# Optimization experiments

Hardware: AMD Instinct MI355X
Metric: run time of the kernel (lower is better)

The kernel has to match this reference:

```python
import jax, jax.numpy as jnp
import numpy as np

FACTOR = 5  # sampling factor from __init__


def setup_inputs() -> dict:
    key = jax.random.key(0)
    k1, k2, k3, k4 = jax.random.split(key, 4)
    B, L, H, D = 4, 2048, 8, 64
    S = min(FACTOR * int(np.ceil(np.log(L))), L)  # U_part = 40
    return {
        "queries": jax.random.normal(k1, (B, L, H, D), jnp.float32),
        "keys": jax.random.normal(k2, (B, L, H, D), jnp.float32),
        "values": jax.random.normal(k3, (B, L, H, D), jnp.float32),
        "index_sample": jax.random.randint(k4, (L, S), 0, L, jnp.int32),
    }


def reference(queries, keys, values, index_sample):
    B, L_Q, H, D = queries.shape
    L_K = keys.shape[1]
    Q = jnp.transpose(queries, (0, 2, 1, 3))  # [B,H,L_Q,D]
    K = jnp.transpose(keys, (0, 2, 1, 3))     # [B,H,L_K,D]
    V = jnp.transpose(values, (0, 2, 1, 3))   # [B,H,L_K,D]

    u = min(FACTOR * int(np.ceil(np.log(L_Q))), L_Q)  # n_top

    # --- _prob_QK: sampled QK to score queries, then top-u query selection ---
    # K_sample[b,h,q,s,:] = K[b,h,index_sample[q,s],:]  -> [B,H,L_Q,S,D]
    K_sample = K[:, :, index_sample, :]
    Q_K_sample = jnp.einsum('bhqd,bhqsd->bhqs', Q, K_sample)  # [B,H,L_Q,S]
    M = Q_K_sample.max(-1) - Q_K_sample.sum(-1) / L_K         # sparsity measure
    _, M_top = jax.lax.top_k(M, u)                            # [B,H,u] query indices

    Q_reduce = jnp.take_along_axis(Q, M_top[..., None], axis=2)  # [B,H,u,D]
    scale = 1.0 / np.sqrt(D)
    scores = jnp.einsum('bhud,bhkd->bhuk', Q_reduce, K) * scale  # [B,H,u,L_K]

    # --- _update_context causal mask: rows are the FIRST u rows of the full
    # triu(L_Q,L_Q) mask (faithful to original, which does NOT reindex by M_top)
    causal = jnp.triu(jnp.ones((u, L_Q), dtype=bool), 1)
    scores = jnp.where(causal[None, None], -jnp.inf, scores)
    attn = jax.nn.softmax(scores, axis=-1)
    upd = jnp.einsum('bhuk,bhkd->bhud', attn, V)  # [B,H,u,D]

    # --- _get_initial_context (mask_flag=True): running cumsum of V ---
    context = jnp.cumsum(V, axis=2)  # [B,H,L_Q,D]

    # scatter-overwrite selected query positions
    b = jnp.arange(B)[:, None, None]
    h = jnp.arange(H)[None, :, None]
    context = context.at[b, h, M_top].set(upd)

    return jnp.transpose(context, (0, 2, 1, 3))  # [B,L_Q,H,D]
```

## Files before the change

### kernel.cpp

```cpp
#include <hip/hip_runtime.h>
#include <stdint.h>

constexpr int B = 4;
constexpr int L = 2048;
constexpr int H = 8;
constexpr int D = 64;
constexpr int S = 40;
constexpr int U = 40;
constexpr int HD = H * D;
constexpr int NSEG = 8;
constexpr int SEGL = L / NSEG;
constexpr int NC = 64;
constexpr int CL = L / NC;

__device__ __forceinline__ unsigned mono(float v) {
    unsigned u = __float_as_uint(v);
    return (u & 0x80000000u) ? ~u : (u | 0x80000000u);
}

typedef float f4v __attribute__((ext_vector_type(4)));

__device__ __forceinline__ float4 ntload4(const float4* p) {
    f4v v = __builtin_nontemporal_load((const f4v*)p);
    return make_float4(v.x, v.y, v.z, v.w);
}

__global__ __launch_bounds__(256) void k_scores(
    const float4* __restrict__ Q4, const float4* __restrict__ K4,
    const int* __restrict__ idxs, float* __restrict__ M)
{
    int i = blockIdx.x;
    int xcd = i & 7;
    int b = xcd >> 1;
    int qc = (i >> 3) * 2 + (xcd & 1);
    int w = threadIdx.x >> 6;
    int lane = threadIdx.x & 63;
    int q = qc * 4 + w;
    int h = lane >> 3;
    int dd = lane & 7;

    const float4* qrow = Q4 + (size_t)(b * L + q) * 128;
    float4 qa = ntload4(qrow + 2 * lane);
    float4 qb = ntload4(qrow + 2 * lane + 1);

    int v_idx = idxs[q * S + (lane < S ? lane : 0)];

    const float4* kbase = K4 + (size_t)b * L * 128;
    float mx = -INFINITY, sm = 0.f;
    #pragma unroll 8
    for (int s = 0; s < S; ++s) {
        int ki = __shfl(v_idx, s);
        const float4* krow = kbase + (size_t)ki * 128;
        float4 ka = krow[2 * lane], kb = krow[2 * lane + 1];
        float d = qa.x * ka.x + qa.y * ka.y + qa.z * ka.z + qa.w * ka.w
                + qb.x * kb.x + qb.y * kb.y + qb.z * kb.z + qb.w * kb.w;
        d += __shfl_xor(d, 1);
        d += __shfl_xor(d, 2);
        d += __shfl_xor(d, 4);
        mx = fmaxf(mx, d);
        sm += d;
    }
    if (dd == 0)
        M[(b * 8 + h) * L + q] = mx - sm * (1.0f / (float)L);
}

__global__ __launch_bounds__(512) void k_topk_attn(
    const float* __restrict__ M, const float4* __restrict__ Q4,
    const float4* __restrict__ K4, const float4* __restrict__ V4,
    int* __restrict__ flags, float* __restrict__ upd)
{
    __shared__ unsigned long long cnd[NSEG * U];
    __shared__ int top_idx[U];
    __shared__ __align__(16) float Qs[U * 68];
    __shared__ __align__(16) float Kst[64 * 65];
    __shared__ __align__(16) float Vs[U * 68];
    __shared__ __align__(16) float Plds[U * 44];

    int bh = blockIdx.x;
    int b = bh >> 3, h = bh & 7;
    int tid = threadIdx.x;
    int wv = tid >> 6, lane = tid & 63;

    int seg = wv;
    int j0 = seg * SEGL + lane * 4;

    *(int4*)(flags + (size_t)bh * L + j0) = make_int4(0, 0, 0, 0);

    float4 v = *(const float4*)(M + (size_t)bh * L + j0);
    unsigned m[4] = { mono(v.x), mono(v.y), mono(v.z), mono(v.w) };
    int rank[4] = { 0, 0, 0, 0 };

    #pragma unroll 4
    for (int src = 0; src < 64; ++src) {
        #pragma unroll
        for (int slot = 0; slot < 4; ++slot) {
            unsigned bm = __shfl(m[slot], src);
            int bj = src * 4 + slot;
            #pragma unroll
            for (int s = 0; s < 4; ++s) {
                int myj = lane * 4 + s;
                rank[s] += (bm > m[s]) || (bm == m[s] && bj < myj);
            }
        }
    }
    #pragma unroll
    for (int s = 0; s < 4; ++s)
        if (rank[s] < U)
            cnd[seg * U + rank[s]] = ((unsigned long long)m[s] << 32)
                                   | (unsigned)(~(unsigned)(j0 + s));
    __syncthreads();

    if (tid < NSEG * U) {
        unsigned long long ka = cnd[tid];
        int ra = 0;
        #pragma unroll 8
        for (int j = 0; j < NSEG * U; ++j) ra += (cnd[j] > ka);
        if (ra < U) top_idx[ra] = (int)(~(unsigned)ka);
    }
    __syncthreads();

    if (tid < U) flags[bh * L + top_idx[tid]] = tid + 1;

    for (int i = tid; i < U * 16; i += 512) {
        int r = i >> 4, d4 = i & 15;
        size_t kvbase = ((size_t)(b * L + r) * H + h) * 16 + d4;
        float4 kv = K4[kvbase];
        Kst[(4 * d4 + 0) * 65 + r] = kv.x;
        Kst[(4 * d4 + 1) * 65 + r] = kv.y;
        Kst[(4 * d4 + 2) * 65 + r] = kv.z;
        Kst[(4 * d4 + 3) * 65 + r] = kv.w;
        *(float4*)(Vs + r * 68 + d4 * 4) = V4[kvbase];
        *(float4*)(Qs + r * 68 + d4 * 4) =
            Q4[((size_t)(b * L + top_idx[r]) * H + h) * 16 + d4];
    }
    __syncthreads();

    const float scale = 0.125f;
    int k = lane;
    for (int rr = 0; rr < 5; ++rr) {
        int r = wv * 5 + rr;
        float acc = 0.f;
        #pragma unroll
        for (int d0 = 0; d0 < D; d0 += 4) {
            float4 qv = *(const float4*)(Qs + r * 68 + d0);
            acc += qv.x * Kst[(d0 + 0) * 65 + k];
            acc += qv.y * Kst[(d0 + 1) * 65 + k];
            acc += qv.z * Kst[(d0 + 2) * 65 + k];
            acc += qv.w * Kst[(d0 + 3) * 65 + k];
        }
        float sc = (k <= r) ? acc * scale : -INFINITY;
        float mx = sc;
        #pragma unroll
        for (int off = 32; off >= 1; off >>= 1)
            mx = fmaxf(mx, __shfl_xor(mx, off));
        float e = __expf(sc - mx);
        float sum = e;
        #pragma unroll
        for (int off = 32; off >= 1; off >>= 1)
            sum += __shfl_xor(sum, off);
        float p = e / sum;
        if (k < U) Plds[r * 44 + k] = p;
    }
    __syncthreads();

    for (int t = tid; t < U * D; t += 512) {
        int r = t >> 6, d = t & 63;
        float acc = 0.f;
        #pragma unroll
        for (int kk = 0; kk < U; kk += 4) {
            float4 pv = *(const float4*)(Plds + r * 44 + kk);
            acc += pv.x * Vs[(kk + 0) * 68 + d];
            acc += pv.y * Vs[(kk + 1) * 68 + d];
            acc += pv.z * Vs[(kk + 2) * 68 + d];
            acc += pv.w * Vs[(kk + 3) * 68 + d];
        }
        upd[((size_t)bh * U + r) * D + d] = acc;
    }
}

__global__ __launch_bounds__(512) void k_chunksum(
    const float* __restrict__ V, float* __restrict__ partial)
{
    int b = blockIdx.x >> 6;
    int c = blockIdx.x & 63;
    int hd = threadIdx.x;
    const float* vp = V + ((size_t)(b * L + c * CL)) * HD + hd;
    float s = 0.f;
    #pragma unroll
    for (int l = 0; l < CL; ++l) s += vp[(size_t)l * HD];
    partial[((size_t)b * NC + c) * HD + hd] = s;
}

__global__ __launch_bounds__(512) void k_out(
    const float* __restrict__ V, const float* __restrict__ partial,
    const int* __restrict__ flags, const float* __restrict__ upd,
    float* __restrict__ out)
{
    int b = blockIdx.x >> 6;
    int c = blockIdx.x & 63;
    int hd = threadIdx.x;
    int h = hd >> 6, d = hd & 63;

    float acc = 0.f;
    const float* pp = partial + (size_t)b * NC * HD + hd;
    for (int j = 0; j < c; ++j) acc += pp[(size_t)j * HD];

    const float* vp = V + ((size_t)(b * L + c * CL)) * HD + hd;
    float*       op = out + ((size_t)(b * L + c * CL)) * HD + hd;
    const int*   fp = flags + (b * H + h) * L + c * CL;
    const float* up = upd + (size_t)(b * H + h) * U * D + d;

    #pragma unroll 4
    for (int l = 0; l < CL; ++l) {
        acc += vp[(size_t)l * HD];
        int f = fp[l];
        float o = f ? up[(size_t)(f - 1) * D] : acc;
        __builtin_nontemporal_store(o, op + (size_t)l * HD);
    }
}

extern "C" void kernel_launch(void* const* d_in, const int* in_sizes, int n_in,
                              void* d_out, int out_size, void* d_ws, size_t ws_size,
                              hipStream_t stream)
{
    const float* Q   = (const float*)d_in[0];
    const float* K   = (const float*)d_in[1];
    const float* V   = (const float*)d_in[2];
    const int*  idxs = (const int*)d_in[3];
    float* out = (float*)d_out;

    char* ws = (char*)d_ws;
    float* M        = (float*)(ws);
    int*   flags    = (int*)  (ws + 262144);
    float* upd      = (float*)(ws + 524288);
    float* partial  = (float*)(ws + 851968);

    k_scores    <<<B * L / 4, 256, 0, stream>>>((const float4*)Q, (const float4*)K, idxs, M);
    k_topk_attn <<<B * H,     512, 0, stream>>>(M, (const float4*)Q, (const float4*)K,
                                                (const float4*)V, flags, upd);
    k_chunksum  <<<B * NC,    512, 0, stream>>>(V, partial);
    k_out       <<<B * NC,    512, 0, stream>>>(V, partial, flags, upd, out);
}
```

Before: 182.4 us.

## Fuse chunk-sum and flag clearing into scores kernel; split top-k across blocks

Merges the V chunk-sum and the flag-zeroing into the scoring kernel's grid as extra block ranges, so those independent jobs run alongside scoring instead of in a later launch. The per-segment rank-based top-k selection moves out of the 32-block attention kernel into its own kernel with 256 small blocks, which writes candidates to global memory. The attention kernel then reloads the candidates and does only the final merge plus attention. This removes one serial phase from the low-parallelism kernel, at the cost of an extra launch and a global round trip for the candidates.

Result: no change. 182.8 us (+0.2%).

```diff
diff --git a/kernel.cpp b/kernel.cpp
--- a/kernel.cpp
+++ b/kernel.cpp
@@ -13,6 +13,10 @@
 constexpr int NC = 64;
 constexpr int CL = L / NC;
 
+constexpr int NBLK_SCORES = B * L / 4;
+constexpr int NBLK_CHUNK  = B * NC;
+constexpr int NBLK_FLAG   = 64;
+
 __device__ __forceinline__ unsigned mono(float v) {
     unsigned u = __float_as_uint(v);
     return (u & 0x80000000u) ? ~u : (u | 0x80000000u);
@@ -25,66 +29,73 @@
     return make_float4(v.x, v.y, v.z, v.w);
 }
 
-__global__ __launch_bounds__(256) void k_scores(
+__global__ __launch_bounds__(256) void k_scores_chunks(
     const float4* __restrict__ Q4, const float4* __restrict__ K4,
-    const int* __restrict__ idxs, float* __restrict__ M)
+    const int* __restrict__ idxs, const float* __restrict__ V,
+    float* __restrict__ M, float* __restrict__ partial,
+    int* __restrict__ flags)
 {
     int i = blockIdx.x;
-    int xcd = i & 7;
-    int b = xcd >> 1;
-    int qc = (i >> 3) * 2 + (xcd & 1);
-    int w = threadIdx.x >> 6;
-    int lane = threadIdx.x & 63;
-    int q = qc * 4 + w;
-    int h = lane >> 3;
-    int dd = lane & 7;
-
-    const float4* qrow = Q4 + (size_t)(b * L + q) * 128;
-    float4 qa = ntload4(qrow + 2 * lane);
-    float4 qb = ntload4(qrow + 2 * lane + 1);
-
-    int v_idx = idxs[q * S + (lane < S ? lane : 0)];
-
-    const float4* kbase = K4 + (size_t)b * L * 128;
-    float mx = -INFINITY, sm = 0.f;
-    #pragma unroll 8
-    for (int s = 0; s < S; ++s) {
-        int ki = __shfl(v_idx, s);
-        const float4* krow = kbase + (size_t)ki * 128;
-        float4 ka = krow[2 * lane], kb = krow[2 * lane + 1];
-        float d = qa.x * ka.x + qa.y * ka.y + qa.z * ka.z + qa.w * ka.w
-                + qb.x * kb.x + qb.y * kb.y + qb.z * kb.z + qb.w * kb.w;
-        d += __shfl_xor(d, 1);
-        d += __shfl_xor(d, 2);
-        d += __shfl_xor(d, 4);
-        mx = fmaxf(mx, d);
-        sm += d;
-    }
-    if (dd == 0)
-        M[(b * 8 + h) * L + q] = mx - sm * (1.0f / (float)L);
-}
-
-__global__ __launch_bounds__(512) void k_topk_attn(
-    const float* __restrict__ M, const float4* __restrict__ Q4,
-    const float4* __restrict__ K4, const float4* __restrict__ V4,
-    int* __restrict__ flags, float* __restrict__ upd)
-{
-    __shared__ unsigned long long cnd[NSEG * U];
-    __shared__ int top_idx[U];
-    __shared__ __align__(16) float Qs[U * 68];
-    __shared__ __align__(16) float Kst[64 * 65];
-    __shared__ __align__(16) float Vs[U * 68];
-    __shared__ __align__(16) float Plds[U * 44];
-
-    int bh = blockIdx.x;
-    int b = bh >> 3, h = bh & 7;
-    int tid = threadIdx.x;
-    int wv = tid >> 6, lane = tid & 63;
-
-    int seg = wv;
+
+    if (i < NBLK_SCORES) {
+        int xcd = i & 7;
+        int b = xcd >> 1;
+        int qc = (i >> 3) * 2 + (xcd & 1);
+        int w = threadIdx.x >> 6;
+        int lane = threadIdx.x & 63;
+        int q = qc * 4 + w;
+        int h = lane >> 3;
+        int dd = lane & 7;
+
+        const float4* qrow = Q4 + (size_t)(b * L + q) * 128;
+        float4 qa = ntload4(qrow + 2 * lane);
+        float4 qb = ntload4(qrow + 2 * lane + 1);
+
+        int v_idx = idxs[q * S + (lane < S ? lane : 0)];
+
+        const float4* kbase = K4 + (size_t)b * L * 128;
+        float mx = -INFINITY, sm = 0.f;
+        #pragma unroll 8
+        for (int s = 0; s < S; ++s) {
+            int ki = __shfl(v_idx, s);
+            const float4* krow = kbase + (size_t)ki * 128;
+            float4 ka = krow[2 * lane], kb = krow[2 * lane + 1];
+            float d = qa.x * ka.x + qa.y * ka.y + qa.z * ka.z + qa.w * ka.w
+                    + qb.x * kb.x + qb.y * kb.y + qb.z * kb.z + qb.w * kb.w;
+            d += __shfl_xor(d, 1);
+            d += __shfl_xor(d, 2);
+            d += __shfl_xor(d, 4);
+            mx = fmaxf(mx, d);
+            sm += d;
+        }
+        if (dd == 0)
+            M[(b * 8 + h) * L + q] = mx - sm * (1.0f / (float)L);
+    } else if (i < NBLK_SCORES + NBLK_CHUNK) {
+        int cidx = i - NBLK_SCORES;
+        int b = cidx >> 6, c = cidx & 63;
+        int t = threadIdx.x;
+        const float* vp = V + ((size_t)(b * L + c * CL)) * HD;
+        float s0 = 0.f, s1 = 0.f;
+        #pragma unroll
+        for (int l = 0; l < CL; ++l) {
+            s0 += __builtin_nontemporal_load(vp + (size_t)l * HD + t);
+            s1 += __builtin_nontemporal_load(vp + (size_t)l * HD + t + 256);
+        }
+        partial[((size_t)b * NC + c) * HD + t]       = s0;
+        partial[((size_t)b * NC + c) * HD + t + 256] = s1;
+    } else {
+        int fidx = i - (NBLK_SCORES + NBLK_CHUNK);
+        ((int4*)flags)[fidx * 256 + threadIdx.x] = make_int4(0, 0, 0, 0);
+    }
+}
+
+__global__ __launch_bounds__(64) void k_seg_topk(
+    const float* __restrict__ M, unsigned long long* __restrict__ cand)
+{
+    int blk = blockIdx.x;
+    int bh = blk >> 3, seg = blk & 7;
+    int lane = threadIdx.x;
     int j0 = seg * SEGL + lane * 4;
-
-    *(int4*)(flags + (size_t)bh * L + j0) = make_int4(0, 0, 0, 0);
 
     float4 v = *(const float4*)(M + (size_t)bh * L + j0);
     unsigned m[4] = { mono(v.x), mono(v.y), mono(v.z), mono(v.w) };
@@ -103,11 +114,34 @@
             }
         }
     }
+
+    unsigned long long* out = cand + (size_t)blk * U;
     #pragma unroll
     for (int s = 0; s < 4; ++s)
         if (rank[s] < U)
-            cnd[seg * U + rank[s]] = ((unsigned long long)m[s] << 32)
-                                   | (unsigned)(~(unsigned)(j0 + s));
+            out[rank[s]] = ((unsigned long long)m[s] << 32)
+                         | (unsigned)(~(unsigned)(j0 + s));
+}
+
+__global__ __launch_bounds__(512) void k_attn(
+    const unsigned long long* __restrict__ cand, const float4* __restrict__ Q4,
+    const float4* __restrict__ K4, const float4* __restrict__ V4,
+    int* __restrict__ flags, float* __restrict__ upd)
+{
+    __shared__ unsigned long long cnd[NSEG * U];
+    __shared__ int top_idx[U];
+    __shared__ __align__(16) float Qs[U * 68];
+    __shared__ __align__(16) float Kst[64 * 65];
+    __shared__ __align__(16) float Vs[U * 68];
+    __shared__ __align__(16) float Plds[U * 44];
+
+    int bh = blockIdx.x;
+    int b = bh >> 3, h = bh & 7;
+    int tid = threadIdx.x;
+    int wv = tid >> 6, lane = tid & 63;
+
+    for (int t = tid; t < NSEG * U; t += 512)
+        cnd[t] = cand[(size_t)bh * NSEG * U + t];
     __syncthreads();
 
     if (tid < NSEG * U) {
@@ -178,19 +212,6 @@
     }
 }
 
-__global__ __launch_bounds__(512) void k_chunksum(
-    const float* __restrict__ V, float* __restrict__ partial)
-{
-    int b = blockIdx.x >> 6;
-    int c = blockIdx.x & 63;
-    int hd = threadIdx.x;
-    const float* vp = V + ((size_t)(b * L + c * CL)) * HD + hd;
-    float s = 0.f;
-    #pragma unroll
-    for (int l = 0; l < CL; ++l) s += vp[(size_t)l * HD];
-    partial[((size_t)b * NC + c) * HD + hd] = s;
-}
-
 __global__ __launch_bounds__(512) void k_out(
     const float* __restrict__ V, const float* __restrict__ partial,
     const int* __restrict__ flags, const float* __restrict__ upd,
@@ -234,10 +255,12 @@
     int*   flags    = (int*)  (ws + 262144);
     float* upd      = (float*)(ws + 524288);
     float* partial  = (float*)(ws + 851968);
-
-    k_scores    <<<B * L / 4, 256, 0, stream>>>((const float4*)Q, (const float4*)K, idxs, M);
-    k_topk_attn <<<B * H,     512, 0, stream>>>(M, (const float4*)Q, (const float4*)K,
-                                                (const float4*)V, flags, upd);
-    k_chunksum  <<<B * NC,    512, 0, stream>>>(V, partial);
-    k_out       <<<B * NC,    512, 0, stream>>>(V, partial, flags, upd, out);
-}
+    unsigned long long* cand = (unsigned long long*)(ws + 1376256);
+
+    k_scores_chunks<<<NBLK_SCORES + NBLK_CHUNK + NBLK_FLAG, 256, 0, stream>>>(
+        (const float4*)Q, (const float4*)K, idxs, V, M, partial, flags);
+    k_seg_topk <<<B * H * NSEG, 64, 0, stream>>>(M, cand);
+    k_attn     <<<B * H,       512, 0, stream>>>(cand, (const float4*)Q, (const float4*)K,
+                                                 (const float4*)V, flags, upd);
+    k_out      <<<B * NC,      512, 0, stream>>>(V, partial, flags, upd, out);
+}
```
